# Kernel optimization log

Hardware: AMD Instinct MI355X
Metric: run time of the kernel (lower is better)

The kernel has to match this reference:

```python
import jax, jax.numpy as jnp
import numpy as np

H = 1024
B = 8192

def setup_inputs() -> dict:
    key = jax.random.key(0)
    ks = jax.random.split(key, 8)
    s = 1.0 / np.sqrt(H)
    return {
        "x": jax.random.normal(ks[0], (B, H), jnp.float32),
        "h": jax.random.normal(ks[1], (B, H), jnp.float32),
        "W_ih_w": jax.random.normal(ks[2], (3 * H, H), jnp.float32) * s,
        "W_ih_b": jax.random.normal(ks[3], (3 * H,), jnp.float32) * s,
        "U_r_w": jax.random.normal(ks[4], (H, H), jnp.float32) * s,
        "U_z_w": jax.random.normal(ks[5], (H, H), jnp.float32) * s,
        "U_n_w": jax.random.normal(ks[6], (H, H), jnp.float32) * s,
        "U_n_b": jax.random.normal(ks[7], (H,), jnp.float32) * s,
    }

def reference(x, h, W_ih_w, W_ih_b, U_r_w, U_z_w, U_n_w, U_n_b):
    # fused input projection: (B, 3H)
    x_proj = x @ W_ih_w.T + W_ih_b
    r_x, z_x, n_x = jnp.split(x_proj, 3, axis=-1)
    # per-gate hidden matmuls (transpose_U=False path)
    r_h = h @ U_r_w.T
    z_h = h @ U_z_w.T
    n_h = h @ U_n_w.T + U_n_b
    r = jax.nn.sigmoid(r_x + r_h)
    z = jax.nn.sigmoid(z_x + z_h)
    n = jnp.tanh(n_x + r * n_h)
    return (1.0 - z) * n + z * h
```

## Files before the change

kernel.cpp:

```cpp
#include <hip/hip_runtime.h>
#include <hip/hip_bf16.h>
#include <cstdint>

#define HDIM 1024
#define NT 32

typedef __attribute__((ext_vector_type(8))) __bf16 bf16x8;
typedef __attribute__((ext_vector_type(8))) unsigned short u16x8;
typedef __attribute__((ext_vector_type(4))) float f32x4;
typedef __attribute__((ext_vector_type(16))) float f32x16;

static __device__ __forceinline__ unsigned short f2b(float f) {
    __hip_bfloat16 h = __float2bfloat16(f);
    return __builtin_bit_cast(unsigned short, h);
}

static __device__ __forceinline__ void barrier_fence() {
    asm volatile("" ::: "memory");
    __builtin_amdgcn_s_barrier();
    asm volatile("" ::: "memory");
}

__global__ void __launch_bounds__(256) cvt_all(
    const float* __restrict__ x, const float* __restrict__ h,
    const float* __restrict__ wih, const float* __restrict__ ur,
    const float* __restrict__ uz, const float* __restrict__ un,
    unsigned short* __restrict__ wb, unsigned short* __restrict__ urb,
    unsigned short* __restrict__ uzb, unsigned short* __restrict__ unb,
    unsigned short* __restrict__ xb, unsigned short* __restrict__ hb) {
    int b = blockIdx.x;
    const float* src; unsigned short* dst; int idx;
    if (b < 3072)       { src = wih; dst = wb;  idx = b; }
    else if (b < 4096)  { src = ur;  dst = urb; idx = b - 3072; }
    else if (b < 5120)  { src = uz;  dst = uzb; idx = b - 4096; }
    else if (b < 6144)  { src = un;  dst = unb; idx = b - 5120; }
    else if (b < 14336) { src = x;   dst = xb;  idx = b - 6144; }
    else                { src = h;   dst = hb;  idx = b - 14336; }
    int i = idx * 256 + threadIdx.x;
    float4 v = ((const float4*)src)[i];
    ushort4 o;
    o.x = f2b(v.x); o.y = f2b(v.y); o.z = f2b(v.z); o.w = f2b(v.w);
    ((ushort4*)dst)[i] = o;
}

__global__ void __launch_bounds__(256, 2)
gru32(const float* __restrict__ hg,
      const unsigned short* __restrict__ xb, const unsigned short* __restrict__ hb,
      const unsigned short* __restrict__ wih,
      const unsigned short* __restrict__ ur,
      const unsigned short* __restrict__ uz,
      const unsigned short* __restrict__ un,
      const float* __restrict__ bih, const float* __restrict__ bun,
      float* __restrict__ out) {
    __shared__ __align__(16) unsigned short smem[2][20480];

    const int tid  = threadIdx.x;
    const int lane = tid & 63;
    const int wv   = tid >> 6;
    const int wm   = wv >> 1;
    const int wn   = wv & 1;
    const int l31  = lane & 31;
    const int lh   = lane >> 5;

    const int bid = blockIdx.x;
    const int swz = (bid & 7) * 128 + (bid >> 3);
    const int m0  = (swz & 63) * 128;
    const int n0  = (swz >> 6) * 64;

    const int wr  = tid >> 2;
    const int wsl = (tid & 3) ^ ((tid >> 3) & 3);
    const unsigned short* pw[6];
    pw[0] = wih + (size_t)(n0 + wr) * HDIM + wsl * 8;
    pw[1] = wih + (size_t)(HDIM + n0 + wr) * HDIM + wsl * 8;
    pw[2] = wih + (size_t)(2 * HDIM + n0 + wr) * HDIM + wsl * 8;
    pw[3] = ur  + (size_t)(n0 + wr) * HDIM + wsl * 8;
    pw[4] = uz  + (size_t)(n0 + wr) * HDIM + wsl * 8;
    pw[5] = un  + (size_t)(n0 + wr) * HDIM + wsl * 8;
    const unsigned short* pxh[4];
#pragma unroll
    for (int half = 0; half < 2; ++half) {
        const int c  = half * 256 + tid;
        const int r  = c >> 2;
        const int sl = (c & 3) ^ ((c >> 3) & 3);
        pxh[half]     = xb + (size_t)(m0 + r) * HDIM + sl * 8;
        pxh[2 + half] = hb + (size_t)(m0 + r) * HDIM + sl * 8;
    }

    const int arow  = wm * 64 + l31;
    const int asel  = (arow >> 1) & 3;
    const int aoff0 = arow * 32 + ((0 + lh) ^ asel) * 8;
    const int aoff1 = arow * 32 + ((2 + lh) ^ asel) * 8;
    const int wrow  = wn * 32 + l31;
    const int bsel  = (wrow >> 1) & 3;
    const int boff0 = 8192 + wrow * 32 + ((0 + lh) ^ bsel) * 8;
    const int boff1 = 8192 + wrow * 32 + ((2 + lh) ^ bsel) * 8;

    f32x16 acc[4][2];
#pragma unroll
    for (int g = 0; g < 4; ++g)
#pragma unroll
        for (int mc = 0; mc < 2; ++mc)
#pragma unroll
            for (int v = 0; v < 16; ++v)
                acc[g][mc][v] = 0.f;

    auto STAGE = [&](int bufi) {
        unsigned short* nb = &smem[bufi][0];
#pragma unroll
        for (int mi = 0; mi < 6; ++mi) {
            __builtin_amdgcn_global_load_lds(
                (const __attribute__((address_space(1))) void*)pw[mi],
                (__attribute__((address_space(3))) void*)(nb + 8192 + mi * 2048 + wv * 512),
                16, 0, 0);
            pw[mi] += 32;
        }
#pragma unroll
        for (int half = 0; half < 2; ++half) {
            __builtin_amdgcn_global_load_lds(
                (const __attribute__((address_space(1))) void*)pxh[half],
                (__attribute__((address_space(3))) void*)(nb + half * 2048 + wv * 512),
                16, 0, 0);
            pxh[half] += 32;
            __builtin_amdgcn_global_load_lds(
                (const __attribute__((address_space(1))) void*)pxh[2 + half],
                (__attribute__((address_space(3))) void*)(nb + 4096 + half * 2048 + wv * 512),
                16, 0, 0);
            pxh[2 + half] += 32;
        }
    };

    auto COMPUTE = [&](int bufi) {
        const unsigned short* sb = &smem[bufi][0];
        bf16x8 ax[2][2], ah[2][2];
#pragma unroll
        for (int mc = 0; mc < 2; ++mc) {
            ax[mc][0] = *(const bf16x8*)(sb + aoff0 + mc * 1024);
            ax[mc][1] = *(const bf16x8*)(sb + aoff1 + mc * 1024);
            ah[mc][0] = *(const bf16x8*)(sb + 4096 + aoff0 + mc * 1024);
            ah[mc][1] = *(const bf16x8*)(sb + 4096 + aoff1 + mc * 1024);
        }
#pragma unroll
        for (int mi = 0; mi < 6; ++mi) {
            bf16x8 b0 = *(const bf16x8*)(sb + boff0 + mi * 2048);
            bf16x8 b1 = *(const bf16x8*)(sb + boff1 + mi * 2048);
            const int g = (mi == 0 || mi == 3) ? 0 : (mi == 1 || mi == 4) ? 1 : (mi == 2) ? 2 : 3;
#pragma unroll
            for (int mc = 0; mc < 2; ++mc) {
                acc[g][mc] = __builtin_amdgcn_mfma_f32_32x32x16_bf16(
                    (mi < 3) ? ax[mc][0] : ah[mc][0], b0, acc[g][mc], 0, 0, 0);
                acc[g][mc] = __builtin_amdgcn_mfma_f32_32x32x16_bf16(
                    (mi < 3) ? ax[mc][1] : ah[mc][1], b1, acc[g][mc], 0, 0, 0);
            }
        }
    };

    auto WAITN = [&]() { asm volatile("s_waitcnt vmcnt(10)" ::: "memory"); };

    STAGE(0);
#pragma unroll 1
    for (int kt = 0; kt < NT - 2; kt += 2) {
        STAGE(1); WAITN(); barrier_fence();
        COMPUTE(0); barrier_fence();
        STAGE(0); WAITN(); barrier_fence();
        COMPUTE(1); barrier_fence();
    }
    STAGE(1); WAITN(); barrier_fence();
    COMPUTE(0); barrier_fence();
    asm volatile("s_waitcnt vmcnt(0) lgkmcnt(0)" ::: "memory");
    __builtin_amdgcn_s_barrier();
    asm volatile("" ::: "memory");
    COMPUTE(1);

    const int gc = n0 + wn * 32 + l31;
    const float br  = bih[gc];
    const float bz  = bih[HDIM + gc];
    const float bnx = bih[2 * HDIM + gc];
    const float bn2 = bun[gc];
#pragma unroll
    for (int mc = 0; mc < 2; ++mc) {
#pragma unroll
        for (int v = 0; v < 16; ++v) {
            const int gr = m0 + wm * 64 + mc * 32 + (v & 3) + 8 * (v >> 2) + 4 * lh;
            const float rv = 1.f / (1.f + __expf(-(acc[0][mc][v] + br)));
            const float zv = 1.f / (1.f + __expf(-(acc[1][mc][v] + bz)));
            const float nv = tanhf(acc[2][mc][v] + bnx + rv * (acc[3][mc][v] + bn2));
            const float hv = hg[(size_t)gr * HDIM + gc];
            out[(size_t)gr * HDIM + gc] = (1.f - zv) * nv + zv * hv;
        }
    }
}

__global__ void __launch_bounds__(256, 2)
gru_fused_fb(const float* __restrict__ hg,
             const float* __restrict__ xg32, const float* __restrict__ hg32,
             const unsigned short* __restrict__ wih,
             const unsigned short* __restrict__ ur,
             const unsigned short* __restrict__ uz,
             const unsigned short* __restrict__ un,
             const float* __restrict__ bih, const float* __restrict__ bun,
             float* __restrict__ out) {
    __shared__ __align__(16) unsigned short smem[2][20480];
    const int tid  = threadIdx.x;
    const int lane = tid & 63;
    const int wv   = tid >> 6;
    const int wm   = wv >> 1;
    const int wn   = wv & 1;
    const int lr   = lane & 15;
    const int ls   = lane >> 4;
    const int m0   = blockIdx.y * 128;
    const int n0   = blockIdx.x * 64;

    const unsigned short* wb6[6] = {
        wih + (size_t)n0 * HDIM, wih + (size_t)(HDIM + n0) * HDIM,
        wih + (size_t)(2 * HDIM + n0) * HDIM, ur + (size_t)n0 * HDIM,
        uz + (size_t)n0 * HDIM, un + (size_t)n0 * HDIM
    };
    const int wr  = tid >> 2;
    const int wsl = (tid & 3) ^ ((tid >> 3) & 3);

    f32x4 acc[4][4][2];
#pragma unroll
    for (int g = 0; g < 4; ++g)
#pragma unroll
        for (int mf = 0; mf < 4; ++mf)
#pragma unroll
            for (int nf = 0; nf < 2; ++nf)
                acc[g][mf][nf] = f32x4{0.f, 0.f, 0.f, 0.f};

    auto STAGE = [&](int bufi, int kt) {
        const int k0 = kt * 32;
        unsigned short* sb = &smem[bufi][0];
        float4 fx[2][2], fh[2][2];
#pragma unroll
        for (int half = 0; half < 2; ++half) {
            const int c2 = half * 256 + tid;
            const int r2 = c2 >> 2;
            const int sl = c2 & 3;
            const float* gx = xg32 + (size_t)(m0 + r2) * HDIM + k0 + sl * 8;
            const float* gh = hg32 + (size_t)(m0 + r2) * HDIM + k0 + sl * 8;
            fx[half][0] = ((const float4*)gx)[0];
            fx[half][1] = ((const float4*)gx)[1];
            fh[half][0] = ((const float4*)gh)[0];
            fh[half][1] = ((const float4*)gh)[1];
        }
#pragma unroll
        for (int mi = 0; mi < 6; ++mi) {
            const unsigned short* g = wb6[mi] + (size_t)wr * HDIM + k0 + wsl * 8;
            __builtin_amdgcn_global_load_lds(
                (const __attribute__((address_space(1))) void*)g,
                (__attribute__((address_space(3))) void*)(sb + 8192 + mi * 2048 + wv * 512),
                16, 0, 0);
        }
#pragma unroll
        for (int half = 0; half < 2; ++half) {
            const int c2 = half * 256 + tid;
            const int r2 = c2 >> 2;
            const int sp = (c2 & 3) ^ ((c2 >> 3) & 3);
            u16x8 px, ph;
#pragma unroll
            for (int q = 0; q < 4; ++q) {
                px[q]     = f2b(fx[half][0][q]);
                px[q + 4] = f2b(fx[half][1][q]);
                ph[q]     = f2b(fh[half][0][q]);
                ph[q + 4] = f2b(fh[half][1][q]);
            }
            *(u16x8*)(sb + r2 * 32 + sp * 8)        = px;
            *(u16x8*)(sb + 4096 + r2 * 32 + sp * 8) = ph;
        }
    };
    auto COMPUTE = [&](int bufi) {
        const unsigned short* sb = &smem[bufi][0];
        const int sel = (lr >> 1) & 3;
        const int fo  = (ls ^ sel) << 3;
        bf16x8 ax[4], ah[4];
#pragma unroll
        for (int mf = 0; mf < 4; ++mf) {
            const int row = wm * 64 + mf * 16 + lr;
            ax[mf] = *(const bf16x8*)(sb + row * 32 + fo);
            ah[mf] = *(const bf16x8*)(sb + 4096 + row * 32 + fo);
        }
#pragma unroll
        for (int mi = 0; mi < 6; ++mi) {
            const unsigned short* wt = sb + 8192 + mi * 2048;
            bf16x8 b0 = *(const bf16x8*)(wt + (wn * 32 + lr) * 32 + fo);
            bf16x8 b1 = *(const bf16x8*)(wt + (wn * 32 + 16 + lr) * 32 + fo);
            const int g = (mi == 0 || mi == 3) ? 0 : (mi == 1 || mi == 4) ? 1 : (mi == 2) ? 2 : 3;
            const bf16x8* a = (mi < 3) ? ax : ah;
#pragma unroll
            for (int mf = 0; mf < 4; ++mf) {
                acc[g][mf][0] = __builtin_amdgcn_mfma_f32_16x16x32_bf16(a[mf], b0, acc[g][mf][0], 0, 0, 0);
                acc[g][mf][1] = __builtin_amdgcn_mfma_f32_16x16x32_bf16(a[mf], b1, acc[g][mf][1], 0, 0, 0);
            }
        }
    };
    auto WAITN = [&]() { asm volatile("s_waitcnt vmcnt(6) lgkmcnt(0)" ::: "memory"); };

    STAGE(0, 0);
#pragma unroll 1
    for (int kt = 0; kt < NT - 2; kt += 2) {
        STAGE(1, kt + 1); WAITN(); barrier_fence();
        COMPUTE(0);       barrier_fence();
        STAGE(0, kt + 2); WAITN(); barrier_fence();
        COMPUTE(1);       barrier_fence();
    }
    STAGE(1, NT - 1); WAITN(); barrier_fence();
    COMPUTE(0);       barrier_fence();
    asm volatile("s_waitcnt vmcnt(0) lgkmcnt(0)" ::: "memory");
    __builtin_amdgcn_s_barrier();
    asm volatile("" ::: "memory");
    COMPUTE(1);

#pragma unroll
    for (int nf = 0; nf < 2; ++nf) {
        const int gc = n0 + wn * 32 + nf * 16 + lr;
        const float br  = bih[gc];
        const float bz  = bih[HDIM + gc];
        const float bnx = bih[2 * HDIM + gc];
        const float bn2 = bun[gc];
#pragma unroll
        for (int mf = 0; mf < 4; ++mf) {
#pragma unroll
            for (int rr = 0; rr < 4; ++rr) {
                const int gr = m0 + wm * 64 + mf * 16 + ls * 4 + rr;
                const float rv = 1.f / (1.f + __expf(-(acc[0][mf][nf][rr] + br)));
                const float zv = 1.f / (1.f + __expf(-(acc[1][mf][nf][rr] + bz)));
                const float nv = tanhf(acc[2][mf][nf][rr] + bnx + rv * (acc[3][mf][nf][rr] + bn2));
                const float hv = hg[(size_t)gr * HDIM + gc];
                out[(size_t)gr * HDIM + gc] = (1.f - zv) * nv + zv * hv;
            }
        }
    }
}

extern "C" void kernel_launch(void* const* d_in, const int* in_sizes, int n_in,
                              void* d_out, int out_size, void* d_ws, size_t ws_size,
                              hipStream_t stream) {
    const float* x   = (const float*)d_in[0];
    const float* h   = (const float*)d_in[1];
    const float* Wih = (const float*)d_in[2];
    const float* bih = (const float*)d_in[3];
    const float* Ur  = (const float*)d_in[4];
    const float* Uz  = (const float*)d_in[5];
    const float* Un  = (const float*)d_in[6];
    const float* bun = (const float*)d_in[7];
    float* out = (float*)d_out;

    unsigned short* wsp  = (unsigned short*)d_ws;
    unsigned short* wihb = wsp;
    unsigned short* urb  = wihb + 3 * 1024 * 1024;
    unsigned short* uzb  = urb + 1024 * 1024;
    unsigned short* unb  = uzb + 1024 * 1024;
    unsigned short* xb   = unb + 1024 * 1024;
    unsigned short* hb   = xb + 8 * 1024 * 1024;

    const bool xhb = ws_size >= 46137344ull;

    cvt_all<<<xhb ? 22528 : 6144, 256, 0, stream>>>(
        x, h, Wih, Ur, Uz, Un, wihb, urb, uzb, unb, xb, hb);

    if (xhb) {
        gru32<<<1024, 256, 0, stream>>>(
            h, xb, hb, wihb, urb, uzb, unb, bih, bun, out);
    } else {
        dim3 grid(HDIM / 64, 8192 / 128);
        gru_fused_fb<<<grid, 256, 0, stream>>>(
            h, x, h, wihb, urb, uzb, unb, bih, bun, out);
    }
}
```

Before: 157.1 us.

## Pack x/h into MFMA fragment layout and load A operands directly to registers

Replaces the combined conversion kernel with a weight-only conversion plus a pack_xh kernel that converts x and h to bf16 and rearranges them into a per-k-tile fragment layout. The main GEMM kernel now uses 512 threads, 16x16x32 MFMAs, and loads A fragments straight from global memory into registers instead of staging them through LDS. Only the weights are staged in shared memory, which cuts LDS traffic and footprint. The cost is an extra LDS transpose pass during packing and more register pressure in the main kernel.

```diff
diff --git a/kernel.cpp b/kernel.cpp
--- a/kernel.cpp
+++ b/kernel.cpp
@@ -8,7 +8,6 @@
 typedef __attribute__((ext_vector_type(8))) __bf16 bf16x8;
 typedef __attribute__((ext_vector_type(8))) unsigned short u16x8;
 typedef __attribute__((ext_vector_type(4))) float f32x4;
-typedef __attribute__((ext_vector_type(16))) float f32x16;
 
 static __device__ __forceinline__ unsigned short f2b(float f) {
     __hip_bfloat16 h = __float2bfloat16(f);
@@ -21,21 +20,17 @@
     asm volatile("" ::: "memory");
 }
 
-__global__ void __launch_bounds__(256) cvt_all(
-    const float* __restrict__ x, const float* __restrict__ h,
+__global__ void __launch_bounds__(256) cvt_w(
     const float* __restrict__ wih, const float* __restrict__ ur,
     const float* __restrict__ uz, const float* __restrict__ un,
     unsigned short* __restrict__ wb, unsigned short* __restrict__ urb,
-    unsigned short* __restrict__ uzb, unsigned short* __restrict__ unb,
-    unsigned short* __restrict__ xb, unsigned short* __restrict__ hb) {
+    unsigned short* __restrict__ uzb, unsigned short* __restrict__ unb) {
     int b = blockIdx.x;
     const float* src; unsigned short* dst; int idx;
     if (b < 3072)       { src = wih; dst = wb;  idx = b; }
     else if (b < 4096)  { src = ur;  dst = urb; idx = b - 3072; }
     else if (b < 5120)  { src = uz;  dst = uzb; idx = b - 4096; }
-    else if (b < 6144)  { src = un;  dst = unb; idx = b - 5120; }
-    else if (b < 14336) { src = x;   dst = xb;  idx = b - 6144; }
-    else                { src = h;   dst = hb;  idx = b - 14336; }
+    else                { src = un;  dst = unb; idx = b - 5120; }
     int i = idx * 256 + threadIdx.x;
     float4 v = ((const float4*)src)[i];
     ushort4 o;
@@ -43,147 +38,170 @@
     ((ushort4*)dst)[i] = o;
 }
 
-__global__ void __launch_bounds__(256, 2)
-gru32(const float* __restrict__ hg,
-      const unsigned short* __restrict__ xb, const unsigned short* __restrict__ hb,
-      const unsigned short* __restrict__ wih,
-      const unsigned short* __restrict__ ur,
-      const unsigned short* __restrict__ uz,
-      const unsigned short* __restrict__ un,
-      const float* __restrict__ bih, const float* __restrict__ bun,
-      float* __restrict__ out) {
-    __shared__ __align__(16) unsigned short smem[2][20480];
+__global__ void __launch_bounds__(256) pack_xh(
+    const float* __restrict__ x, const float* __restrict__ h,
+    unsigned short* __restrict__ xf, unsigned short* __restrict__ hf) {
+    __shared__ unsigned short lds[16 * 1032];
+    const int b = blockIdx.x;
+    const float* src = (b < 512) ? x : h;
+    unsigned short* dst = (b < 512) ? xf : hf;
+    const int f = b & 511;
+    const int tid = threadIdx.x;
+
+#pragma unroll
+    for (int rep = 0; rep < 4; ++rep) {
+        const int idx  = rep * 256 + tid;
+        const int row  = idx >> 6;
+        const int colg = (idx & 63) * 16;
+        const float* g = src + (size_t)(f * 16 + row) * HDIM + colg;
+        float4 v0 = ((const float4*)g)[0];
+        float4 v1 = ((const float4*)g)[1];
+        float4 v2 = ((const float4*)g)[2];
+        float4 v3 = ((const float4*)g)[3];
+        unsigned short* l = lds + row * 1032 + colg;
+        l[0]=f2b(v0.x); l[1]=f2b(v0.y); l[2]=f2b(v0.z); l[3]=f2b(v0.w);
+        l[4]=f2b(v1.x); l[5]=f2b(v1.y); l[6]=f2b(v1.z); l[7]=f2b(v1.w);
+        l[8]=f2b(v2.x); l[9]=f2b(v2.y); l[10]=f2b(v2.z); l[11]=f2b(v2.w);
+        l[12]=f2b(v3.x); l[13]=f2b(v3.y); l[14]=f2b(v3.z); l[15]=f2b(v3.w);
+    }
+    __syncthreads();
+
+#pragma unroll
+    for (int rep = 0; rep < 8; ++rep) {
+        const int idx = rep * 256 + tid;
+        const int kt  = idx >> 6;
+        const int l   = idx & 63;
+        u16x8 v = *(const u16x8*)(lds + (l & 15) * 1032 + kt * 32 + (l >> 4) * 8);
+        *(u16x8*)(dst + ((size_t)(kt * 512 + f) * 64 + l) * 8) = v;
+    }
+}
+
+__global__ void __launch_bounds__(512, 2)
+gru8(const float* __restrict__ hg,
+     const unsigned short* __restrict__ xf, const unsigned short* __restrict__ hf,
+     const unsigned short* __restrict__ wih,
+     const unsigned short* __restrict__ ur,
+     const unsigned short* __restrict__ uz,
+     const unsigned short* __restrict__ un,
+     const float* __restrict__ bih, const float* __restrict__ bun,
+     float* __restrict__ out) {
+    __shared__ __align__(16) unsigned short smem[2][12288];
 
     const int tid  = threadIdx.x;
     const int lane = tid & 63;
     const int wv   = tid >> 6;
-    const int wm   = wv >> 1;
-    const int wn   = wv & 1;
-    const int l31  = lane & 31;
-    const int lh   = lane >> 5;
-
-    const int bid = blockIdx.x;
-    const int swz = (bid & 7) * 128 + (bid >> 3);
-    const int m0  = (swz & 63) * 128;
-    const int n0  = (swz >> 6) * 64;
-
-    const int wr  = tid >> 2;
-    const int wsl = (tid & 3) ^ ((tid >> 3) & 3);
-    const unsigned short* pw[6];
-    pw[0] = wih + (size_t)(n0 + wr) * HDIM + wsl * 8;
-    pw[1] = wih + (size_t)(HDIM + n0 + wr) * HDIM + wsl * 8;
-    pw[2] = wih + (size_t)(2 * HDIM + n0 + wr) * HDIM + wsl * 8;
-    pw[3] = ur  + (size_t)(n0 + wr) * HDIM + wsl * 8;
-    pw[4] = uz  + (size_t)(n0 + wr) * HDIM + wsl * 8;
-    pw[5] = un  + (size_t)(n0 + wr) * HDIM + wsl * 8;
-    const unsigned short* pxh[4];
-#pragma unroll
-    for (int half = 0; half < 2; ++half) {
-        const int c  = half * 256 + tid;
+    const int mo   = wv >> 2;
+    const int no   = wv & 3;
+    const int lr   = lane & 15;
+    const int ls   = lane >> 4;
+
+    const int bid  = blockIdx.x;
+    const int swz  = (bid & 7) * 128 + (bid >> 3);
+    const int m0   = (swz & 63) * 128;
+    const int n0   = (swz >> 6) * 64;
+
+    const unsigned short* wb6[6] = {
+        wih + (size_t)n0 * HDIM,
+        wih + (size_t)(HDIM + n0) * HDIM,
+        wih + (size_t)(2 * HDIM + n0) * HDIM,
+        ur  + (size_t)n0 * HDIM,
+        uz  + (size_t)n0 * HDIM,
+        un  + (size_t)n0 * HDIM
+    };
+    const unsigned short* pwp[3];
+    int ldst[3];
+#pragma unroll
+    for (int l = 0; l < 3; ++l) {
+        const int id = l * 512 + tid;
+        const int mi = id >> 8;
+        const int c  = id & 255;
         const int r  = c >> 2;
         const int sl = (c & 3) ^ ((c >> 3) & 3);
-        pxh[half]     = xb + (size_t)(m0 + r) * HDIM + sl * 8;
-        pxh[2 + half] = hb + (size_t)(m0 + r) * HDIM + sl * 8;
-    }
-
-    const int arow  = wm * 64 + l31;
-    const int asel  = (arow >> 1) & 3;
-    const int aoff0 = arow * 32 + ((0 + lh) ^ asel) * 8;
-    const int aoff1 = arow * 32 + ((2 + lh) ^ asel) * 8;
-    const int wrow  = wn * 32 + l31;
-    const int bsel  = (wrow >> 1) & 3;
-    const int boff0 = 8192 + wrow * 32 + ((0 + lh) ^ bsel) * 8;
-    const int boff1 = 8192 + wrow * 32 + ((2 + lh) ^ bsel) * 8;
-
-    f32x16 acc[4][2];
+        pwp[l]  = wb6[mi] + (size_t)r * HDIM + sl * 8;
+        ldst[l] = mi * 2048 + (wv & 3) * 512;
+    }
+
+    const int fbx = (m0 >> 4) + mo * 4;
+    const unsigned short* pxA = xf + ((size_t)fbx * 64 + lane) * 8;
+    const unsigned short* phA = hf + ((size_t)fbx * 64 + lane) * 8;
+
+    f32x4 acc[4][4];
 #pragma unroll
     for (int g = 0; g < 4; ++g)
 #pragma unroll
-        for (int mc = 0; mc < 2; ++mc)
-#pragma unroll
-            for (int v = 0; v < 16; ++v)
-                acc[g][mc][v] = 0.f;
-
-    auto STAGE = [&](int bufi) {
-        unsigned short* nb = &smem[bufi][0];
+        for (int mf = 0; mf < 4; ++mf)
+            acc[g][mf] = f32x4{0.f, 0.f, 0.f, 0.f};
+
+    bf16x8 ax0[4], ah0[4], ax1[4], ah1[4];
+
+    auto STAGE_W = [&](unsigned short* nb) {
+#pragma unroll
+        for (int l = 0; l < 3; ++l) {
+            __builtin_amdgcn_global_load_lds(
+                (const __attribute__((address_space(1))) void*)pwp[l],
+                (__attribute__((address_space(3))) void*)(nb + ldst[l]), 16, 0, 0);
+            pwp[l] += 32;
+        }
+    };
+    auto A_LOAD = [&](bf16x8 (&ax)[4], bf16x8 (&ah)[4]) {
+#pragma unroll
+        for (int mf = 0; mf < 4; ++mf) ax[mf] = *(const bf16x8*)(pxA + mf * 512);
+#pragma unroll
+        for (int mf = 0; mf < 4; ++mf) ah[mf] = *(const bf16x8*)(phA + mf * 512);
+        pxA += 262144; phA += 262144;
+    };
+    auto COMPUTE = [&](const unsigned short* sb,
+                       const bf16x8 (&ax)[4], const bf16x8 (&ah)[4]) {
+        const int wrow = no * 16 + lr;
+        const int boff = wrow * 32 + ((ls ^ ((wrow >> 1) & 3)) << 3);
 #pragma unroll
         for (int mi = 0; mi < 6; ++mi) {
-            __builtin_amdgcn_global_load_lds(
-                (const __attribute__((address_space(1))) void*)pw[mi],
-                (__attribute__((address_space(3))) void*)(nb + 8192 + mi * 2048 + wv * 512),
-                16, 0, 0);
-            pw[mi] += 32;
-        }
-#pragma unroll
-        for (int half = 0; half < 2; ++half) {
-            __builtin_amdgcn_global_load_lds(
-                (const __attribute__((address_space(1))) void*)pxh[half],
-                (__attribute__((address_space(3))) void*)(nb + half * 2048 + wv * 512),
-                16, 0, 0);
-            pxh[half] += 32;
-            __builtin_amdgcn_global_load_lds(
-                (const __attribute__((address_space(1))) void*)pxh[2 + half],
-                (__attribute__((address_space(3))) void*)(nb + 4096 + half * 2048 + wv * 512),
-                16, 0, 0);
-            pxh[2 + half] += 32;
-        }
-    };
-
-    auto COMPUTE = [&](int bufi) {
-        const unsigned short* sb = &smem[bufi][0];
-        bf16x8 ax[2][2], ah[2][2];
-#pragma unroll
-        for (int mc = 0; mc < 2; ++mc) {
-            ax[mc][0] = *(const bf16x8*)(sb + aoff0 + mc * 1024);
-            ax[mc][1] = *(const bf16x8*)(sb + aoff1 + mc * 1024);
-            ah[mc][0] = *(const bf16x8*)(sb + 4096 + aoff0 + mc * 1024);
-            ah[mc][1] = *(const bf16x8*)(sb + 4096 + aoff1 + mc * 1024);
-        }
-#pragma unroll
-        for (int mi = 0; mi < 6; ++mi) {
-            bf16x8 b0 = *(const bf16x8*)(sb + boff0 + mi * 2048);
-            bf16x8 b1 = *(const bf16x8*)(sb + boff1 + mi * 2048);
+            bf16x8 bq = *(const bf16x8*)(sb + mi * 2048 + boff);
             const int g = (mi == 0 || mi == 3) ? 0 : (mi == 1 || mi == 4) ? 1 : (mi == 2) ? 2 : 3;
-#pragma unroll
-            for (int mc = 0; mc < 2; ++mc) {
-                acc[g][mc] = __builtin_amdgcn_mfma_f32_32x32x16_bf16(
-                    (mi < 3) ? ax[mc][0] : ah[mc][0], b0, acc[g][mc], 0, 0, 0);
-                acc[g][mc] = __builtin_amdgcn_mfma_f32_32x32x16_bf16(
-                    (mi < 3) ? ax[mc][1] : ah[mc][1], b1, acc[g][mc], 0, 0, 0);
-            }
-        }
-    };
-
-    auto WAITN = [&]() { asm volatile("s_waitcnt vmcnt(10)" ::: "memory"); };
-
-    STAGE(0);
+            const bf16x8* a = (mi < 3) ? ax : ah;
+#pragma unroll
+            for (int mf = 0; mf < 4; ++mf)
+                acc[g][mf] = __builtin_amdgcn_mfma_f32_16x16x32_bf16(a[mf], bq, acc[g][mf], 0, 0, 0);
+        }
+    };
+    auto WAIT11 = [&]() { asm volatile("s_waitcnt vmcnt(11)" ::: "memory"); };
+
+    STAGE_W(&smem[0][0]);
+    A_LOAD(ax0, ah0);
+
 #pragma unroll 1
-    for (int kt = 0; kt < NT - 2; kt += 2) {
-        STAGE(1); WAITN(); barrier_fence();
-        COMPUTE(0); barrier_fence();
-        STAGE(0); WAITN(); barrier_fence();
-        COMPUTE(1); barrier_fence();
-    }
-    STAGE(1); WAITN(); barrier_fence();
-    COMPUTE(0); barrier_fence();
+    for (int t = 0; t < NT - 2; t += 2) {
+        STAGE_W(&smem[1][0]); A_LOAD(ax1, ah1);
+        WAIT11(); barrier_fence();
+        COMPUTE(&smem[0][0], ax0, ah0);
+        barrier_fence();
+        STAGE_W(&smem[0][0]); A_LOAD(ax0, ah0);
+        WAIT11(); barrier_fence();
+        COMPUTE(&smem[1][0], ax1, ah1);
+        barrier_fence();
+    }
+    STAGE_W(&smem[1][0]); A_LOAD(ax1, ah1);
+    WAIT11(); barrier_fence();
+    COMPUTE(&smem[0][0], ax0, ah0);
+    barrier_fence();
     asm volatile("s_waitcnt vmcnt(0) lgkmcnt(0)" ::: "memory");
     __builtin_amdgcn_s_barrier();
     asm volatile("" ::: "memory");
-    COMPUTE(1);
-
-    const int gc = n0 + wn * 32 + l31;
+    COMPUTE(&smem[1][0], ax1, ah1);
+
+    const int gc = n0 + no * 16 + lr;
     const float br  = bih[gc];
     const float bz  = bih[HDIM + gc];
     const float bnx = bih[2 * HDIM + gc];
     const float bn2 = bun[gc];
 #pragma unroll
-    for (int mc = 0; mc < 2; ++mc) {
-#pragma unroll
-        for (int v = 0; v < 16; ++v) {
-            const int gr = m0 + wm * 64 + mc * 32 + (v & 3) + 8 * (v >> 2) + 4 * lh;
-            const float rv = 1.f / (1.f + __expf(-(acc[0][mc][v] + br)));
-            const float zv = 1.f / (1.f + __expf(-(acc[1][mc][v] + bz)));
-            const float nv = tanhf(acc[2][mc][v] + bnx + rv * (acc[3][mc][v] + bn2));
+    for (int mf = 0; mf < 4; ++mf) {
+#pragma unroll
+        for (int rr = 0; rr < 4; ++rr) {
+            const int gr = m0 + mo * 64 + mf * 16 + ls * 4 + rr;
+            const float rv = 1.f / (1.f + __expf(-(acc[0][mf][rr] + br)));
+            const float zv = 1.f / (1.f + __expf(-(acc[1][mf][rr] + bz)));
+            const float nv = tanhf(acc[2][mf][rr] + bnx + rv * (acc[3][mf][rr] + bn2));
             const float hv = hg[(size_t)gr * HDIM + gc];
             out[(size_t)gr * HDIM + gc] = (1.f - zv) * nv + zv * hv;
         }
@@ -350,17 +368,17 @@
     unsigned short* urb  = wihb + 3 * 1024 * 1024;
     unsigned short* uzb  = urb + 1024 * 1024;
     unsigned short* unb  = uzb + 1024 * 1024;
-    unsigned short* xb   = unb + 1024 * 1024;
-    unsigned short* hb   = xb + 8 * 1024 * 1024;
-
-    const bool xhb = ws_size >= 46137344ull;
-
-    cvt_all<<<xhb ? 22528 : 6144, 256, 0, stream>>>(
-        x, h, Wih, Ur, Uz, Un, wihb, urb, uzb, unb, xb, hb);
-
-    if (xhb) {
-        gru32<<<1024, 256, 0, stream>>>(
-            h, xb, hb, wihb, urb, uzb, unb, bih, bun, out);
+    unsigned short* xff  = unb + 1024 * 1024;
+    unsigned short* hff  = xff + 8 * 1024 * 1024;
+
+    const bool big = ws_size >= 46137344ull;
+
+    cvt_w<<<6144, 256, 0, stream>>>(Wih, Ur, Uz, Un, wihb, urb, uzb, unb);
+
+    if (big) {
+        pack_xh<<<1024, 256, 0, stream>>>(x, h, xff, hff);
+        gru8<<<1024, 512, 0, stream>>>(
+            h, xff, hff, wihb, urb, uzb, unb, bih, bun, out);
     } else {
         dim3 grid(HDIM / 64, 8192 / 128);
         gru_fused_fb<<<grid, 256, 0, stream>>>(
```

Result: slower. 199.8 us (+27.2%).

## Switch GRU GEMM to 16x16x32 MFMA tiles with XCD-aware panel mapping

Applied to the files above, without the earlier changes.

Replaces the 32x32x16 bf16 MFMA with 16x16x32 fragments (4x2 per warp per gate), changing the LDS read pattern and accumulator layout. The block-to-tile mapping now assigns each XCD two contiguous weight column panels, aiming for better L2 reuse of weights. Global addresses are recomputed from kt instead of kept as incremented pointers, and the wait count is raised. The epilogue reads h from the bf16 copy instead of fp32, cutting epilogue traffic but mixing bf16-rounded h into the output blend, which lowers accuracy.

```diff
diff --git a/kernel.cpp b/kernel.cpp
--- a/kernel.cpp
+++ b/kernel.cpp
@@ -8,11 +8,14 @@
 typedef __attribute__((ext_vector_type(8))) __bf16 bf16x8;
 typedef __attribute__((ext_vector_type(8))) unsigned short u16x8;
 typedef __attribute__((ext_vector_type(4))) float f32x4;
-typedef __attribute__((ext_vector_type(16))) float f32x16;
 
 static __device__ __forceinline__ unsigned short f2b(float f) {
     __hip_bfloat16 h = __float2bfloat16(f);
     return __builtin_bit_cast(unsigned short, h);
+}
+static __device__ __forceinline__ float b2f(unsigned short u) {
+    unsigned int w = ((unsigned int)u) << 16;
+    return __builtin_bit_cast(float, w);
 }
 
 static __device__ __forceinline__ void barrier_fence() {
@@ -44,14 +47,13 @@
 }
 
 __global__ void __launch_bounds__(256, 2)
-gru32(const float* __restrict__ hg,
-      const unsigned short* __restrict__ xb, const unsigned short* __restrict__ hb,
-      const unsigned short* __restrict__ wih,
-      const unsigned short* __restrict__ ur,
-      const unsigned short* __restrict__ uz,
-      const unsigned short* __restrict__ un,
-      const float* __restrict__ bih, const float* __restrict__ bun,
-      float* __restrict__ out) {
+gru7(const unsigned short* __restrict__ xb, const unsigned short* __restrict__ hb,
+     const unsigned short* __restrict__ wih,
+     const unsigned short* __restrict__ ur,
+     const unsigned short* __restrict__ uz,
+     const unsigned short* __restrict__ un,
+     const float* __restrict__ bih, const float* __restrict__ bun,
+     float* __restrict__ out) {
     __shared__ __align__(16) unsigned short smem[2][20480];
 
     const int tid  = threadIdx.x;
@@ -59,133 +61,127 @@
     const int wv   = tid >> 6;
     const int wm   = wv >> 1;
     const int wn   = wv & 1;
-    const int l31  = lane & 31;
-    const int lh   = lane >> 5;
-
-    const int bid = blockIdx.x;
-    const int swz = (bid & 7) * 128 + (bid >> 3);
-    const int m0  = (swz & 63) * 128;
-    const int n0  = (swz >> 6) * 64;
+    const int lr   = lane & 15;
+    const int ls   = lane >> 4;
+
+    const int bid   = blockIdx.x;
+    const int xcd   = bid & 7;
+    const int loc   = bid >> 3;
+    const int panel = xcd * 2 + (loc >> 6);
+    const int m0    = (loc & 63) * 128;
+    const int n0    = panel * 64;
+
+    const unsigned short* wb6[6] = {
+        wih + (size_t)n0 * HDIM,
+        wih + (size_t)(HDIM + n0) * HDIM,
+        wih + (size_t)(2 * HDIM + n0) * HDIM,
+        ur  + (size_t)n0 * HDIM,
+        uz  + (size_t)n0 * HDIM,
+        un  + (size_t)n0 * HDIM
+    };
 
     const int wr  = tid >> 2;
     const int wsl = (tid & 3) ^ ((tid >> 3) & 3);
-    const unsigned short* pw[6];
-    pw[0] = wih + (size_t)(n0 + wr) * HDIM + wsl * 8;
-    pw[1] = wih + (size_t)(HDIM + n0 + wr) * HDIM + wsl * 8;
-    pw[2] = wih + (size_t)(2 * HDIM + n0 + wr) * HDIM + wsl * 8;
-    pw[3] = ur  + (size_t)(n0 + wr) * HDIM + wsl * 8;
-    pw[4] = uz  + (size_t)(n0 + wr) * HDIM + wsl * 8;
-    pw[5] = un  + (size_t)(n0 + wr) * HDIM + wsl * 8;
-    const unsigned short* pxh[4];
-#pragma unroll
-    for (int half = 0; half < 2; ++half) {
-        const int c  = half * 256 + tid;
-        const int r  = c >> 2;
-        const int sl = (c & 3) ^ ((c >> 3) & 3);
-        pxh[half]     = xb + (size_t)(m0 + r) * HDIM + sl * 8;
-        pxh[2 + half] = hb + (size_t)(m0 + r) * HDIM + sl * 8;
-    }
-
-    const int arow  = wm * 64 + l31;
-    const int asel  = (arow >> 1) & 3;
-    const int aoff0 = arow * 32 + ((0 + lh) ^ asel) * 8;
-    const int aoff1 = arow * 32 + ((2 + lh) ^ asel) * 8;
-    const int wrow  = wn * 32 + l31;
-    const int bsel  = (wrow >> 1) & 3;
-    const int boff0 = 8192 + wrow * 32 + ((0 + lh) ^ bsel) * 8;
-    const int boff1 = 8192 + wrow * 32 + ((2 + lh) ^ bsel) * 8;
-
-    f32x16 acc[4][2];
+
+    f32x4 acc[4][4][2];
 #pragma unroll
     for (int g = 0; g < 4; ++g)
 #pragma unroll
-        for (int mc = 0; mc < 2; ++mc)
-#pragma unroll
-            for (int v = 0; v < 16; ++v)
-                acc[g][mc][v] = 0.f;
-
-    auto STAGE = [&](int bufi) {
-        unsigned short* nb = &smem[bufi][0];
+        for (int mf = 0; mf < 4; ++mf)
+#pragma unroll
+            for (int nf = 0; nf < 2; ++nf)
+                acc[g][mf][nf] = f32x4{0.f, 0.f, 0.f, 0.f};
+
+    auto STAGE = [&](int bufi, int kt) {
+        const int k0 = kt * 32;
+        unsigned short* sb = &smem[bufi][0];
 #pragma unroll
         for (int mi = 0; mi < 6; ++mi) {
+            const unsigned short* g = wb6[mi] + (size_t)wr * HDIM + k0 + wsl * 8;
             __builtin_amdgcn_global_load_lds(
-                (const __attribute__((address_space(1))) void*)pw[mi],
-                (__attribute__((address_space(3))) void*)(nb + 8192 + mi * 2048 + wv * 512),
+                (const __attribute__((address_space(1))) void*)g,
+                (__attribute__((address_space(3))) void*)(sb + 8192 + mi * 2048 + wv * 512),
                 16, 0, 0);
-            pw[mi] += 32;
         }
 #pragma unroll
         for (int half = 0; half < 2; ++half) {
+            const int c2 = half * 256 + tid;
+            const int r2 = c2 >> 2;
+            const int sl = (c2 & 3) ^ ((c2 >> 3) & 3);
+            const unsigned short* gx = xb + (size_t)(m0 + r2) * HDIM + k0 + sl * 8;
+            const unsigned short* gh = hb + (size_t)(m0 + r2) * HDIM + k0 + sl * 8;
             __builtin_amdgcn_global_load_lds(
-                (const __attribute__((address_space(1))) void*)pxh[half],
-                (__attribute__((address_space(3))) void*)(nb + half * 2048 + wv * 512),
+                (const __attribute__((address_space(1))) void*)gx,
+                (__attribute__((address_space(3))) void*)(sb + half * 2048 + wv * 512),
                 16, 0, 0);
-            pxh[half] += 32;
             __builtin_amdgcn_global_load_lds(
-                (const __attribute__((address_space(1))) void*)pxh[2 + half],
-                (__attribute__((address_space(3))) void*)(nb + 4096 + half * 2048 + wv * 512),
+                (const __attribute__((address_space(1))) void*)gh,
+                (__attribute__((address_space(3))) void*)(sb + 4096 + half * 2048 + wv * 512),
                 16, 0, 0);
-            pxh[2 + half] += 32;
         }
     };
 
     auto COMPUTE = [&](int bufi) {
         const unsigned short* sb = &smem[bufi][0];
-        bf16x8 ax[2][2], ah[2][2];
-#pragma unroll
-        for (int mc = 0; mc < 2; ++mc) {
-            ax[mc][0] = *(const bf16x8*)(sb + aoff0 + mc * 1024);
-            ax[mc][1] = *(const bf16x8*)(sb + aoff1 + mc * 1024);
-            ah[mc][0] = *(const bf16x8*)(sb + 4096 + aoff0 + mc * 1024);
-            ah[mc][1] = *(const bf16x8*)(sb + 4096 + aoff1 + mc * 1024);
+        const int sel = (lr >> 1) & 3;
+        const int fo  = (ls ^ sel) << 3;
+        bf16x8 ax[4], ah[4];
+#pragma unroll
+        for (int mf = 0; mf < 4; ++mf) {
+            const int row = wm * 64 + mf * 16 + lr;
+            ax[mf] = *(const bf16x8*)(sb + row * 32 + fo);
+            ah[mf] = *(const bf16x8*)(sb + 4096 + row * 32 + fo);
         }
 #pragma unroll
         for (int mi = 0; mi < 6; ++mi) {
-            bf16x8 b0 = *(const bf16x8*)(sb + boff0 + mi * 2048);
-            bf16x8 b1 = *(const bf16x8*)(sb + boff1 + mi * 2048);
+            const unsigned short* wt = sb + 8192 + mi * 2048;
+            bf16x8 b0 = *(const bf16x8*)(wt + (wn * 32 + lr) * 32 + fo);
+            bf16x8 b1 = *(const bf16x8*)(wt + (wn * 32 + 16 + lr) * 32 + fo);
             const int g = (mi == 0 || mi == 3) ? 0 : (mi == 1 || mi == 4) ? 1 : (mi == 2) ? 2 : 3;
-#pragma unroll
-            for (int mc = 0; mc < 2; ++mc) {
-                acc[g][mc] = __builtin_amdgcn_mfma_f32_32x32x16_bf16(
-                    (mi < 3) ? ax[mc][0] : ah[mc][0], b0, acc[g][mc], 0, 0, 0);
-                acc[g][mc] = __builtin_amdgcn_mfma_f32_32x32x16_bf16(
-                    (mi < 3) ? ax[mc][1] : ah[mc][1], b1, acc[g][mc], 0, 0, 0);
-            }
-        }
-    };
-
-    auto WAITN = [&]() { asm volatile("s_waitcnt vmcnt(10)" ::: "memory"); };
-
-    STAGE(0);
+            const bf16x8* a = (mi < 3) ? ax : ah;
+#pragma unroll
+            for (int mf = 0; mf < 4; ++mf) {
+                acc[g][mf][0] = __builtin_amdgcn_mfma_f32_16x16x32_bf16(a[mf], b0, acc[g][mf][0], 0, 0, 0);
+                acc[g][mf][1] = __builtin_amdgcn_mfma_f32_16x16x32_bf16(a[mf], b1, acc[g][mf][1], 0, 0, 0);
+            }
+        }
+    };
+
+    auto WAITN = [&]() { asm volatile("s_waitcnt vmcnt(14)" ::: "memory"); };
+
+    STAGE(0, 0);
 #pragma unroll 1
     for (int kt = 0; kt < NT - 2; kt += 2) {
-        STAGE(1); WAITN(); barrier_fence();
-        COMPUTE(0); barrier_fence();
-        STAGE(0); WAITN(); barrier_fence();
-        COMPUTE(1); barrier_fence();
-    }
-    STAGE(1); WAITN(); barrier_fence();
-    COMPUTE(0); barrier_fence();
+        STAGE(1, kt + 1); WAITN(); barrier_fence();
+        COMPUTE(0);       barrier_fence();
+        STAGE(0, kt + 2); WAITN(); barrier_fence();
+        COMPUTE(1);       barrier_fence();
+    }
+    STAGE(1, NT - 1); WAITN(); barrier_fence();
+    COMPUTE(0);       barrier_fence();
     asm volatile("s_waitcnt vmcnt(0) lgkmcnt(0)" ::: "memory");
     __builtin_amdgcn_s_barrier();
     asm volatile("" ::: "memory");
     COMPUTE(1);
 
-    const int gc = n0 + wn * 32 + l31;
-    const float br  = bih[gc];
-    const float bz  = bih[HDIM + gc];
-    const float bnx = bih[2 * HDIM + gc];
-    const float bn2 = bun[gc];
-#pragma unroll
-    for (int mc = 0; mc < 2; ++mc) {
-#pragma unroll
-        for (int v = 0; v < 16; ++v) {
-            const int gr = m0 + wm * 64 + mc * 32 + (v & 3) + 8 * (v >> 2) + 4 * lh;
-            const float rv = 1.f / (1.f + __expf(-(acc[0][mc][v] + br)));
-            const float zv = 1.f / (1.f + __expf(-(acc[1][mc][v] + bz)));
-            const float nv = tanhf(acc[2][mc][v] + bnx + rv * (acc[3][mc][v] + bn2));
-            const float hv = hg[(size_t)gr * HDIM + gc];
-            out[(size_t)gr * HDIM + gc] = (1.f - zv) * nv + zv * hv;
+#pragma unroll
+    for (int nf = 0; nf < 2; ++nf) {
+        const int gc = n0 + wn * 32 + nf * 16 + lr;
+        const float br  = bih[gc];
+        const float bz  = bih[HDIM + gc];
+        const float bnx = bih[2 * HDIM + gc];
+        const float bn2 = bun[gc];
+#pragma unroll
+        for (int mf = 0; mf < 4; ++mf) {
+#pragma unroll
+            for (int rr = 0; rr < 4; ++rr) {
+                const int gr = m0 + wm * 64 + mf * 16 + ls * 4 + rr;
+                const float rv = 1.f / (1.f + __expf(-(acc[0][mf][nf][rr] + br)));
+                const float zv = 1.f / (1.f + __expf(-(acc[1][mf][nf][rr] + bz)));
+                const float nv = tanhf(acc[2][mf][nf][rr] + bnx + rv * (acc[3][mf][nf][rr] + bn2));
+                const float hv = b2f(hb[(size_t)gr * HDIM + gc]);
+                out[(size_t)gr * HDIM + gc] = (1.f - zv) * nv + zv * hv;
+            }
         }
     }
 }
@@ -350,17 +346,17 @@
     unsigned short* urb  = wihb + 3 * 1024 * 1024;
     unsigned short* uzb  = urb + 1024 * 1024;
     unsigned short* unb  = uzb + 1024 * 1024;
-    unsigned short* xb   = unb + 1024 * 1024;
-    unsigned short* hb   = xb + 8 * 1024 * 1024;
-
-    const bool xhb = ws_size >= 46137344ull;
-
-    cvt_all<<<xhb ? 22528 : 6144, 256, 0, stream>>>(
-        x, h, Wih, Ur, Uz, Un, wihb, urb, uzb, unb, xb, hb);
-
-    if (xhb) {
-        gru32<<<1024, 256, 0, stream>>>(
-            h, xb, hb, wihb, urb, uzb, unb, bih, bun, out);
+    unsigned short* xbb  = unb + 1024 * 1024;
+    unsigned short* hbb  = xbb + 8 * 1024 * 1024;
+
+    const bool big = ws_size >= 46137344ull;
+
+    cvt_all<<<big ? 22528 : 6144, 256, 0, stream>>>(
+        x, h, Wih, Ur, Uz, Un, wihb, urb, uzb, unb, xbb, hbb);
+
+    if (big) {
+        gru7<<<1024, 256, 0, stream>>>(
+            xbb, hbb, wihb, urb, uzb, unb, bih, bun, out);
     } else {
         dim3 grid(HDIM / 64, 8192 / 128);
         gru_fused_fb<<<grid, 256, 0, stream>>>(
```

New measurement: 155.4 us. No clear change (-1.1%).
